# Kernel optimization log

Measured on AMD Instinct MI355X. Metric: run time of the kernel, lower is better.

Reference implementation:

```python
import jax, jax.numpy as jnp
import numpy as np

N = 524288          # number of query points
L_FREQ = 16         # frequencies in positional encoding -> dim_encoding = 3*2*16 = 96
DIM_ENC = 96
DIM_HID = 128
NUM_LAYERS = 8      # 1 input layer + 7 hidden layers + 1 output layer
DIM_OUT = 4
DIM_IN_HID = DIM_HID + DIM_ENC  # concat skip: 224


def setup_inputs() -> dict:
    key = jax.random.key(0)
    ks = jax.random.split(key, 7)
    def lin(k, fan_in, shape):
        return jax.random.uniform(k, shape, jnp.float32, -1.0, 1.0) / np.sqrt(fan_in)
    return {
        "query_points": jax.random.uniform(ks[0], (N, 3), jnp.float32),
        "W0": lin(ks[1], DIM_ENC, (DIM_ENC, DIM_HID)),
        "b0": lin(ks[2], DIM_ENC, (DIM_HID,)),
        "Wh": lin(ks[3], DIM_IN_HID, (NUM_LAYERS - 1, DIM_IN_HID, DIM_HID)),
        "bh": lin(ks[4], DIM_IN_HID, (NUM_LAYERS - 1, DIM_HID)),
        "Wl": lin(ks[5], DIM_IN_HID, (DIM_IN_HID, DIM_OUT)),
        "bl": lin(ks[6], DIM_IN_HID, (DIM_OUT,)),
    }


def _encode(x):
    # NeRF frequency encoding: [N,3] -> [N, 3*2*L_FREQ]
    freqs = (2.0 ** jnp.arange(L_FREQ, dtype=x.dtype)) * jnp.pi
    xf = x[..., None] * freqs                      # [N, 3, L]
    enc = jnp.concatenate([jnp.sin(xf), jnp.cos(xf)], axis=-1)  # [N, 3, 2L]
    return enc.reshape(x.shape[0], -1)             # [N, 96]


def reference(query_points, W0, b0, Wh, bh, Wl, bl):
    enc = _encode(query_points)                    # [N, 96]
    outs = jnp.maximum(enc @ W0 + b0, 0.0)         # [N, 128]
    outs = jnp.concatenate([outs, enc], axis=-1)   # concat skip -> [N, 224]
    for i in range(Wh.shape[0]):                   # 7 structurally-distinct hidden layers
        outs = jnp.maximum(outs @ Wh[i] + bh[i], 0.0)
        outs = jnp.concatenate([outs, enc], axis=-1)
    return outs @ Wl + bl                          # [N, 4], no activation on last layer
```

## Files before the change

kernel.cpp:

```cpp
#include <hip/hip_runtime.h>
#include <stdint.h>

typedef unsigned short u16;
typedef __bf16 bf16x8 __attribute__((ext_vector_type(8)));
typedef float f32x4 __attribute__((ext_vector_type(4)));
typedef float f32x16 __attribute__((ext_vector_type(16)));
typedef unsigned int u32;

#define IMG_H(l) (14336 + ((l)-1) * 30720)
#define IMG_OUT 229376
#define IMG_TOTAL 237056

__device__ inline int fmap(int k) {
    int s = k >> 4, h = (k >> 3) & 1, j = k & 7;
    return 32 * (s >> 1) + 16 * (s & 1) + 8 * (j >> 2) + 4 * h + (j & 3);
}
__device__ inline u16 b16rne(float v) {
    u32 u = __builtin_bit_cast(u32, v);
    u += 0x7FFFu + ((u >> 16) & 1u);
    return (u16)(u >> 16);
}

__global__ void nf_prep(const float* __restrict__ W0, const float* __restrict__ b0,
                        const float* __restrict__ Wh, const float* __restrict__ bh,
                        const float* __restrict__ Wl, const float* __restrict__ bl,
                        u16* __restrict__ img) {
    int idx = blockIdx.x * 256 + threadIdx.x;
    if (idx >= IMG_TOTAL) return;
    float v;
    if (idx < 14336) {
        int gg = idx >> 3, j = idx & 7;
        int koct = gg >> 7, i = gg & 127, k = koct * 8 + j;
        v = (k < 96) ? W0[k * 128 + i] : (k == 96) ? b0[i] : 0.f;
    } else if (idx < IMG_OUT) {
        int r = idx - 14336, l = r / 30720, rr = r % 30720;
        int gg = rr >> 3, j = rr & 7;
        int koct = gg >> 7, i = gg & 127, k = koct * 8 + j;
        const float* W = Wh + l * 224 * 128;
        v = (k < 128) ? W[fmap(k) * 128 + i]
          : (k < 224) ? W[k * 128 + i]
          : (k == 224) ? bh[l * 128 + i] : 0.f;
    } else {
        int r = idx - IMG_OUT;
        int gg = r >> 3, j = r & 7;
        int koct = gg >> 5, i = gg & 31, k = koct * 8 + j;
        v = 0.f;
        if (i < 4)
            v = (k < 128) ? Wl[fmap(k) * 4 + i]
              : (k < 224) ? Wl[k * 4 + i]
              : (k == 224) ? bl[i] : 0.f;
    }
    img[idx] = b16rne(v);
}

__device__ inline f32x16 MF32(bf16x8 a, bf16x8 b, f32x16 c) {
    return __builtin_amdgcn_mfma_f32_32x32x16_bf16(a, b, c, 0, 0, 0);
}
__device__ inline bf16x8 fr4(const u32 (&p)[4]) {
    union { u32 u[4]; bf16x8 v; } x;
    x.u[0] = p[0]; x.u[1] = p[1]; x.u[2] = p[2]; x.u[3] = p[3];
    return x.v;
}
__device__ inline bf16x8 frCB(u32 c0) {
    union { u32 u[4]; bf16x8 v; } x;
    x.u[0] = c0; x.u[1] = 0; x.u[2] = 0; x.u[3] = 0;
    return x.v;
}
__device__ inline bf16x8 ldA(const u16* base, int gi) {
    union { uint4 q; bf16x8 v; } x;
    x.q = *(const uint4*)(base + (gi << 3));
    return x.v;
}
__device__ inline u32 pkbf(float a, float b) {
    u32 ua = __builtin_bit_cast(u32, a) + 0x8000u;
    u32 ub = __builtin_bit_cast(u32, b) + 0x8000u;
    return __builtin_amdgcn_perm(ub, ua, 0x07060302u);
}
__device__ inline void stageA(const u16* gsrc, u16* ldst, int bytes, int wave, int lane) {
    const char* gs = (const char*)gsrc + lane * 16;
    char* ls = (char*)ldst;
    for (int c = wave * 1024; c < bytes; c += 4096)
        __builtin_amdgcn_global_load_lds(
            (const __attribute__((address_space(1))) void*)(gs + c),
            (__attribute__((address_space(3))) void*)(ls + c), 16, 0, 0);
}
__device__ inline void zeroacc(f32x16 (&acc)[4][2]) {
#pragma unroll
    for (int t = 0; t < 4; t++)
#pragma unroll
        for (int n = 0; n < 2; n++)
#pragma unroll
            for (int r = 0; r < 16; r++) acc[t][n][r] = 0.f;
}
__device__ inline void buildH(const f32x16 (&acc)[4][2], u32 (&H)[2][8][4]) {
#pragma unroll
    for (int n = 0; n < 2; n++)
#pragma unroll
        for (int s = 0; s < 8; s++) {
            const int t = s >> 1, rb = (s & 1) * 8;
#pragma unroll
            for (int q = 0; q < 4; q++)
                H[n][s][q] = pkbf(fmaxf(acc[t][n][rb + 2 * q], 0.f),
                                  fmaxf(acc[t][n][rb + 2 * q + 1], 0.f));
        }
}

#define WAITV(N) asm volatile("s_waitcnt vmcnt(" #N ")" ::: "memory")
#define BAR() do { __builtin_amdgcn_s_barrier(); __builtin_amdgcn_sched_barrier(0); } while (0)

__device__ inline void mmRow(const u16* A, int h, int m32, int s,
                             bf16x8 B0, bf16x8 B1, f32x16 (&acc)[4][2]) {
#pragma unroll
    for (int t = 0; t < 4; t++) {
        bf16x8 a = ldA(A, (2 * s + h) * 128 + t * 32 + m32);
        acc[t][0] = MF32(a, B0, acc[t][0]);
        acc[t][1] = MF32(a, B1, acc[t][1]);
    }
}

__device__ inline void cH04(const u16* A, int h, int m32, f32x16 (&acc)[4][2],
                            const u32 (&H)[2][8][4]) {
    __builtin_amdgcn_s_setprio(1);
#pragma unroll
    for (int s = 0; s < 5; s++)
        mmRow(A, h, m32, s, fr4(H[0][s]), fr4(H[1][s]), acc);
    __builtin_amdgcn_s_setprio(0);
}
__device__ inline void cH57E0(const u16* A, int h, int m32, f32x16 (&acc)[4][2],
                              const u32 (&H)[2][8][4], const u32 (&E)[2][3][2][4]) {
    __builtin_amdgcn_s_setprio(1);
    mmRow(A, h, m32, 0, fr4(H[0][5]), fr4(H[1][5]), acc);
    mmRow(A, h, m32, 1, fr4(H[0][6]), fr4(H[1][6]), acc);
    mmRow(A, h, m32, 2, fr4(H[0][7]), fr4(H[1][7]), acc);
    mmRow(A, h, m32, 3, fr4(E[0][0][0]), fr4(E[1][0][0]), acc);
    mmRow(A, h, m32, 4, fr4(E[0][0][1]), fr4(E[1][0][1]), acc);
    __builtin_amdgcn_s_setprio(0);
}
__device__ inline void cE12b(const u16* A, int h, int m32, f32x16 (&acc)[4][2],
                             const u32 (&E)[2][3][2][4], u32 CB0) {
    __builtin_amdgcn_s_setprio(1);
    mmRow(A, h, m32, 0, fr4(E[0][1][0]), fr4(E[1][1][0]), acc);
    mmRow(A, h, m32, 1, fr4(E[0][1][1]), fr4(E[1][1][1]), acc);
    mmRow(A, h, m32, 2, fr4(E[0][2][0]), fr4(E[1][2][0]), acc);
    mmRow(A, h, m32, 3, fr4(E[0][2][1]), fr4(E[1][2][1]), acc);
    mmRow(A, h, m32, 4, frCB(CB0), frCB(CB0), acc);
    __builtin_amdgcn_s_setprio(0);
}
__device__ inline void cL0a(const u16* A, int h, int m32, f32x16 (&acc)[4][2],
                            const u32 (&E)[2][3][2][4]) {
    __builtin_amdgcn_s_setprio(1);
#pragma unroll
    for (int s = 0; s < 5; s++)
        mmRow(A, h, m32, s, fr4(E[0][s >> 1][s & 1]), fr4(E[1][s >> 1][s & 1]), acc);
    __builtin_amdgcn_s_setprio(0);
}
__device__ inline void cL0b(const u16* A, int h, int m32, f32x16 (&acc)[4][2],
                            const u32 (&E)[2][3][2][4], u32 CB0) {
    __builtin_amdgcn_s_setprio(1);
    mmRow(A, h, m32, 0, fr4(E[0][2][1]), fr4(E[1][2][1]), acc);
    mmRow(A, h, m32, 1, frCB(CB0), frCB(CB0), acc);
    __builtin_amdgcn_s_setprio(0);
}

__global__ __launch_bounds__(256, 2) void nf_main(const float* __restrict__ qp,
                                                  const u16* __restrict__ img,
                                                  float* __restrict__ out) {
    __shared__ alignas(16) u16 lds[3][10240];
    const int tid = threadIdx.x, wave = tid >> 6, lane = tid & 63;
    const int m32 = lane & 31, h = lane >> 5;
    const int pbase = blockIdx.x * 256 + wave * 64;

    stageA(img, &lds[0][0], 20480, wave, lane);
    stageA(img + 10240, &lds[1][0], 8192, wave, lane);

    u32 E[2][3][2][4];
    const float sc0 = h ? 128.0f : 0.5f;
#pragma unroll
    for (int n = 0; n < 2; n++)
#pragma unroll
        for (int c = 0; c < 3; c++) {
            float r = qp[(pbase + n * 32 + m32) * 3 + c] * sc0;
            float sn[8], cs[8];
#pragma unroll
            for (int t = 0; t < 8; t++) {
                float fr = __builtin_amdgcn_fractf(r);
                sn[t] = __builtin_amdgcn_sinf(fr);
                cs[t] = __builtin_amdgcn_cosf(fr);
                r = r * 2.0f;
            }
#pragma unroll
            for (int q = 0; q < 4; q++) {
                E[n][c][0][q] = pkbf(sn[2 * q], sn[2 * q + 1]);
                E[n][c][1][q] = pkbf(cs[2 * q], cs[2 * q + 1]);
            }
        }
    const u32 CB0 = (h == 0) ? 0x00003F80u : 0u;

    f32x16 acc[4][2];
    u32 H[2][8][4];
    zeroacc(acc);

    WAITV(2); BAR();
    stageA(img + IMG_H(1), &lds[2][0], 20480, wave, lane);
    cL0a(&lds[0][0], h, m32, acc, E);
    WAITV(5); BAR();
    stageA(img + IMG_H(1) + 10240, &lds[0][0], 20480, wave, lane);
    cL0b(&lds[1][0], h, m32, acc, E, CB0);
    buildH(acc, H);
    WAITV(5); BAR();

#pragma unroll 1
    for (int l = 1; l < 8; l++) {
        const int base = IMG_H(l);
        stageA(img + base + 20480, &lds[1][0], 20480, wave, lane);
        zeroacc(acc);
        cH04(&lds[2][0], h, m32, acc, H);
        WAITV(5); BAR();
        const u16* nsrc = (l < 7) ? (img + IMG_H(l + 1)) : (img + IMG_OUT);
        stageA(nsrc, &lds[2][0], (l < 7) ? 20480 : 15360, wave, lane);
        cH57E0(&lds[0][0], h, m32, acc, H, E);
        if (l < 7) { WAITV(5); } else { WAITV(3); }
        BAR();
        if (l < 7)
            stageA(img + IMG_H(l + 1) + 10240, &lds[0][0], 20480, wave, lane);
        cE12b(&lds[1][0], h, m32, acc, E, CB0);
        buildH(acc, H);
        if (l < 7) { WAITV(5); } else { WAITV(0); }
        BAR();
    }

    f32x16 o0, o1;
#pragma unroll
    for (int r = 0; r < 16; r++) { o0[r] = 0.f; o1[r] = 0.f; }
    __builtin_amdgcn_s_setprio(1);
#pragma unroll
    for (int s = 0; s < 15; s++) {
        bf16x8 B0, B1;
        if (s < 8)       { B0 = fr4(H[0][s]); B1 = fr4(H[1][s]); }
        else if (s < 14) { B0 = fr4(E[0][(s - 8) >> 1][(s - 8) & 1]);
                           B1 = fr4(E[1][(s - 8) >> 1][(s - 8) & 1]); }
        else             { B0 = frCB(CB0); B1 = B0; }
        bf16x8 a = ldA(&lds[2][0], (2 * s + h) * 32 + m32);
        o0 = MF32(a, B0, o0);
        o1 = MF32(a, B1, o1);
    }
    __builtin_amdgcn_s_setprio(0);
    if (h == 0) {
        f32x4 w0 = {o0[0], o0[1], o0[2], o0[3]};
        f32x4 w1 = {o1[0], o1[1], o1[2], o1[3]};
        *(f32x4*)(out + 4 * (pbase + m32)) = w0;
        *(f32x4*)(out + 4 * (pbase + 32 + m32)) = w1;
    }
}

extern "C" void kernel_launch(void* const* d_in, const int* in_sizes, int n_in,
                              void* d_out, int out_size, void* d_ws, size_t ws_size,
                              hipStream_t stream) {
    const float* qp = (const float*)d_in[0];
    const float* W0 = (const float*)d_in[1];
    const float* b0 = (const float*)d_in[2];
    const float* Wh = (const float*)d_in[3];
    const float* bh = (const float*)d_in[4];
    const float* Wl = (const float*)d_in[5];
    const float* bl = (const float*)d_in[6];
    float* out = (float*)d_out;
    u16* img = (u16*)d_ws;

    nf_prep<<<926, 256, 0, stream>>>(W0, b0, Wh, bh, Wl, bl, img);
    nf_main<<<2048, 256, 0, stream>>>(qp, img, out);
}
```

Measured before the change: 261.7 us.

## Halve points per wave to cut registers and run three blocks per CU

Each wave now processes 32 points instead of 64, which halves the accumulator and activation register footprint. Launch bounds go from 2 to 3 blocks per CU and the grid doubles. The weight staging is restructured into 16 KB chunks that rotate through a triple LDS buffer with pointer swaps. It also adds an s_sleep on alternating blocks to stagger their start. The trade-off is that each weight fragment loaded from LDS now feeds one MFMA instead of two, so LDS traffic per FLOP doubles.

```diff
diff --git a/kernel.cpp b/kernel.cpp
--- a/kernel.cpp
+++ b/kernel.cpp
@@ -84,172 +84,162 @@
             (const __attribute__((address_space(1))) void*)(gs + c),
             (__attribute__((address_space(3))) void*)(ls + c), 16, 0, 0);
 }
-__device__ inline void zeroacc(f32x16 (&acc)[4][2]) {
+__device__ inline void zeroacc(f32x16 (&acc)[4]) {
 #pragma unroll
     for (int t = 0; t < 4; t++)
 #pragma unroll
-        for (int n = 0; n < 2; n++)
-#pragma unroll
-            for (int r = 0; r < 16; r++) acc[t][n][r] = 0.f;
-}
-__device__ inline void buildH(const f32x16 (&acc)[4][2], u32 (&H)[2][8][4]) {
-#pragma unroll
-    for (int n = 0; n < 2; n++)
-#pragma unroll
-        for (int s = 0; s < 8; s++) {
-            const int t = s >> 1, rb = (s & 1) * 8;
-#pragma unroll
-            for (int q = 0; q < 4; q++)
-                H[n][s][q] = pkbf(fmaxf(acc[t][n][rb + 2 * q], 0.f),
-                                  fmaxf(acc[t][n][rb + 2 * q + 1], 0.f));
-        }
+        for (int r = 0; r < 16; r++) acc[t][r] = 0.f;
+}
+__device__ inline void buildH(const f32x16 (&acc)[4], u32 (&H)[8][4]) {
+#pragma unroll
+    for (int s = 0; s < 8; s++) {
+        const int t = s >> 1, rb = (s & 1) * 8;
+#pragma unroll
+        for (int q = 0; q < 4; q++)
+            H[s][q] = pkbf(fmaxf(acc[t][rb + 2 * q], 0.f),
+                           fmaxf(acc[t][rb + 2 * q + 1], 0.f));
+    }
 }
 
 #define WAITV(N) asm volatile("s_waitcnt vmcnt(" #N ")" ::: "memory")
 #define BAR() do { __builtin_amdgcn_s_barrier(); __builtin_amdgcn_sched_barrier(0); } while (0)
 
-__device__ inline void mmRow(const u16* A, int h, int m32, int s,
-                             bf16x8 B0, bf16x8 B1, f32x16 (&acc)[4][2]) {
+__device__ inline void mmS(const u16* A, int h, int m32, int sl,
+                           bf16x8 B0, f32x16 (&acc)[4]) {
 #pragma unroll
     for (int t = 0; t < 4; t++) {
-        bf16x8 a = ldA(A, (2 * s + h) * 128 + t * 32 + m32);
-        acc[t][0] = MF32(a, B0, acc[t][0]);
-        acc[t][1] = MF32(a, B1, acc[t][1]);
-    }
-}
-
-__device__ inline void cH04(const u16* A, int h, int m32, f32x16 (&acc)[4][2],
-                            const u32 (&H)[2][8][4]) {
-    __builtin_amdgcn_s_setprio(1);
-#pragma unroll
-    for (int s = 0; s < 5; s++)
-        mmRow(A, h, m32, s, fr4(H[0][s]), fr4(H[1][s]), acc);
-    __builtin_amdgcn_s_setprio(0);
-}
-__device__ inline void cH57E0(const u16* A, int h, int m32, f32x16 (&acc)[4][2],
-                              const u32 (&H)[2][8][4], const u32 (&E)[2][3][2][4]) {
-    __builtin_amdgcn_s_setprio(1);
-    mmRow(A, h, m32, 0, fr4(H[0][5]), fr4(H[1][5]), acc);
-    mmRow(A, h, m32, 1, fr4(H[0][6]), fr4(H[1][6]), acc);
-    mmRow(A, h, m32, 2, fr4(H[0][7]), fr4(H[1][7]), acc);
-    mmRow(A, h, m32, 3, fr4(E[0][0][0]), fr4(E[1][0][0]), acc);
-    mmRow(A, h, m32, 4, fr4(E[0][0][1]), fr4(E[1][0][1]), acc);
-    __builtin_amdgcn_s_setprio(0);
-}
-__device__ inline void cE12b(const u16* A, int h, int m32, f32x16 (&acc)[4][2],
-                             const u32 (&E)[2][3][2][4], u32 CB0) {
-    __builtin_amdgcn_s_setprio(1);
-    mmRow(A, h, m32, 0, fr4(E[0][1][0]), fr4(E[1][1][0]), acc);
-    mmRow(A, h, m32, 1, fr4(E[0][1][1]), fr4(E[1][1][1]), acc);
-    mmRow(A, h, m32, 2, fr4(E[0][2][0]), fr4(E[1][2][0]), acc);
-    mmRow(A, h, m32, 3, fr4(E[0][2][1]), fr4(E[1][2][1]), acc);
-    mmRow(A, h, m32, 4, frCB(CB0), frCB(CB0), acc);
-    __builtin_amdgcn_s_setprio(0);
-}
-__device__ inline void cL0a(const u16* A, int h, int m32, f32x16 (&acc)[4][2],
-                            const u32 (&E)[2][3][2][4]) {
-    __builtin_amdgcn_s_setprio(1);
-#pragma unroll
-    for (int s = 0; s < 5; s++)
-        mmRow(A, h, m32, s, fr4(E[0][s >> 1][s & 1]), fr4(E[1][s >> 1][s & 1]), acc);
-    __builtin_amdgcn_s_setprio(0);
-}
-__device__ inline void cL0b(const u16* A, int h, int m32, f32x16 (&acc)[4][2],
-                            const u32 (&E)[2][3][2][4], u32 CB0) {
-    __builtin_amdgcn_s_setprio(1);
-    mmRow(A, h, m32, 0, fr4(E[0][2][1]), fr4(E[1][2][1]), acc);
-    mmRow(A, h, m32, 1, frCB(CB0), frCB(CB0), acc);
-    __builtin_amdgcn_s_setprio(0);
-}
-
-__global__ __launch_bounds__(256, 2) void nf_main(const float* __restrict__ qp,
+        bf16x8 a = ldA(A, (2 * sl + h) * 128 + t * 32 + m32);
+        acc[t] = MF32(a, B0, acc[t]);
+    }
+}
+
+__device__ inline void phH03(const u16* A, int h, int m32, f32x16 (&acc)[4],
+                             const u32 (&H)[8][4]) {
+    __builtin_amdgcn_s_setprio(1);
+#pragma unroll
+    for (int sl = 0; sl < 4; sl++) mmS(A, h, m32, sl, fr4(H[sl]), acc);
+    __builtin_amdgcn_s_setprio(0);
+}
+__device__ inline void phH47(const u16* A, int h, int m32, f32x16 (&acc)[4],
+                             const u32 (&H)[8][4]) {
+    __builtin_amdgcn_s_setprio(1);
+#pragma unroll
+    for (int sl = 0; sl < 4; sl++) mmS(A, h, m32, sl, fr4(H[4 + sl]), acc);
+    __builtin_amdgcn_s_setprio(0);
+}
+__device__ inline void phE01(const u16* A, int h, int m32, f32x16 (&acc)[4],
+                             const u32 (&E)[3][2][4]) {
+    __builtin_amdgcn_s_setprio(1);
+#pragma unroll
+    for (int sl = 0; sl < 4; sl++)
+        mmS(A, h, m32, sl, fr4(E[sl >> 1][sl & 1]), acc);
+    __builtin_amdgcn_s_setprio(0);
+}
+__device__ inline void phE2b(const u16* A, int h, int m32, f32x16 (&acc)[4],
+                             const u32 (&E)[3][2][4], u32 CB0) {
+    __builtin_amdgcn_s_setprio(1);
+    mmS(A, h, m32, 0, fr4(E[2][0]), acc);
+    mmS(A, h, m32, 1, fr4(E[2][1]), acc);
+    mmS(A, h, m32, 2, frCB(CB0), acc);
+    __builtin_amdgcn_s_setprio(0);
+}
+
+__global__ __launch_bounds__(256, 3) void nf_main(const float* __restrict__ qp,
                                                   const u16* __restrict__ img,
                                                   float* __restrict__ out) {
-    __shared__ alignas(16) u16 lds[3][10240];
+    __shared__ alignas(16) u16 lds[3][8192];
     const int tid = threadIdx.x, wave = tid >> 6, lane = tid & 63;
     const int m32 = lane & 31, h = lane >> 5;
-    const int pbase = blockIdx.x * 256 + wave * 64;
-
-    stageA(img, &lds[0][0], 20480, wave, lane);
-    stageA(img + 10240, &lds[1][0], 8192, wave, lane);
-
-    u32 E[2][3][2][4];
+    const int pbase = blockIdx.x * 128 + wave * 32;
+
+    if ((blockIdx.x ^ (blockIdx.x >> 8)) & 1) __builtin_amdgcn_s_sleep(20);
+
+    u16* p0 = &lds[0][0];
+    u16* p1 = &lds[1][0];
+    u16* p2 = &lds[2][0];
+
+    stageA(img, p0, 16384, wave, lane);
+    stageA(img + 8192, p1, 12288, wave, lane);
+
+    u32 E[3][2][4];
     const float sc0 = h ? 128.0f : 0.5f;
 #pragma unroll
-    for (int n = 0; n < 2; n++)
-#pragma unroll
-        for (int c = 0; c < 3; c++) {
-            float r = qp[(pbase + n * 32 + m32) * 3 + c] * sc0;
-            float sn[8], cs[8];
-#pragma unroll
-            for (int t = 0; t < 8; t++) {
-                float fr = __builtin_amdgcn_fractf(r);
-                sn[t] = __builtin_amdgcn_sinf(fr);
-                cs[t] = __builtin_amdgcn_cosf(fr);
-                r = r * 2.0f;
-            }
-#pragma unroll
-            for (int q = 0; q < 4; q++) {
-                E[n][c][0][q] = pkbf(sn[2 * q], sn[2 * q + 1]);
-                E[n][c][1][q] = pkbf(cs[2 * q], cs[2 * q + 1]);
-            }
+    for (int c = 0; c < 3; c++) {
+        float r = qp[(pbase + m32) * 3 + c] * sc0;
+        float sn[8], cs[8];
+#pragma unroll
+        for (int t = 0; t < 8; t++) {
+            float fr = __builtin_amdgcn_fractf(r);
+            sn[t] = __builtin_amdgcn_sinf(fr);
+            cs[t] = __builtin_amdgcn_cosf(fr);
+            r = r * 2.0f;
         }
+#pragma unroll
+        for (int q = 0; q < 4; q++) {
+            E[c][0][q] = pkbf(sn[2 * q], sn[2 * q + 1]);
+            E[c][1][q] = pkbf(cs[2 * q], cs[2 * q + 1]);
+        }
+    }
     const u32 CB0 = (h == 0) ? 0x00003F80u : 0u;
 
-    f32x16 acc[4][2];
-    u32 H[2][8][4];
+    f32x16 acc[4];
+    u32 H[8][4];
     zeroacc(acc);
 
-    WAITV(2); BAR();
-    stageA(img + IMG_H(1), &lds[2][0], 20480, wave, lane);
-    cL0a(&lds[0][0], h, m32, acc, E);
-    WAITV(5); BAR();
-    stageA(img + IMG_H(1) + 10240, &lds[0][0], 20480, wave, lane);
-    cL0b(&lds[1][0], h, m32, acc, E, CB0);
+    WAITV(3); BAR();
+    stageA(img + IMG_H(1), p2, 16384, wave, lane);
+    phE01(p0, h, m32, acc, E);
+    WAITV(4); BAR();
+    { u16* t = p0; p0 = p1; p1 = p2; p2 = t; }
+    stageA(img + IMG_H(1) + 8192, p2, 16384, wave, lane);
+    phE2b(p0, h, m32, acc, E, CB0);
     buildH(acc, H);
-    WAITV(5); BAR();
+    WAITV(4); BAR();
+    { u16* t = p0; p0 = p1; p1 = p2; p2 = t; }
 
 #pragma unroll 1
     for (int l = 1; l < 8; l++) {
         const int base = IMG_H(l);
-        stageA(img + base + 20480, &lds[1][0], 20480, wave, lane);
+        stageA(img + base + 16384, p2, 16384, wave, lane);
         zeroacc(acc);
-        cH04(&lds[2][0], h, m32, acc, H);
-        WAITV(5); BAR();
-        const u16* nsrc = (l < 7) ? (img + IMG_H(l + 1)) : (img + IMG_OUT);
-        stageA(nsrc, &lds[2][0], (l < 7) ? 20480 : 15360, wave, lane);
-        cH57E0(&lds[0][0], h, m32, acc, H, E);
-        if (l < 7) { WAITV(5); } else { WAITV(3); }
+        phH03(p0, h, m32, acc, H);
+        WAITV(4); BAR();
+        { u16* t = p0; p0 = p1; p1 = p2; p2 = t; }
+        stageA(img + base + 24576, p2, 12288, wave, lane);
+        phH47(p0, h, m32, acc, H);
+        WAITV(3); BAR();
+        { u16* t = p0; p0 = p1; p1 = p2; p2 = t; }
+        if (l < 7) stageA(img + IMG_H(l + 1), p2, 16384, wave, lane);
+        else       stageA(img + IMG_OUT, p2, 15360, wave, lane);
+        phE01(p0, h, m32, acc, E);
+        if (l < 7) { WAITV(4); } else { WAITV(3); }
         BAR();
-        if (l < 7)
-            stageA(img + IMG_H(l + 1) + 10240, &lds[0][0], 20480, wave, lane);
-        cE12b(&lds[1][0], h, m32, acc, E, CB0);
+        { u16* t = p0; p0 = p1; p1 = p2; p2 = t; }
+        if (l < 7) stageA(img + IMG_H(l + 1) + 8192, p2, 16384, wave, lane);
+        phE2b(p0, h, m32, acc, E, CB0);
         buildH(acc, H);
-        if (l < 7) { WAITV(5); } else { WAITV(0); }
+        if (l < 7) { WAITV(4); } else { WAITV(0); }
         BAR();
-    }
-
-    f32x16 o0, o1;
-#pragma unroll
-    for (int r = 0; r < 16; r++) { o0[r] = 0.f; o1[r] = 0.f; }
+        { u16* t = p0; p0 = p1; p1 = p2; p2 = t; }
+    }
+
+    f32x16 o0;
+#pragma unroll
+    for (int r = 0; r < 16; r++) o0[r] = 0.f;
     __builtin_amdgcn_s_setprio(1);
 #pragma unroll
     for (int s = 0; s < 15; s++) {
-        bf16x8 B0, B1;
-        if (s < 8)       { B0 = fr4(H[0][s]); B1 = fr4(H[1][s]); }
-        else if (s < 14) { B0 = fr4(E[0][(s - 8) >> 1][(s - 8) & 1]);
-                           B1 = fr4(E[1][(s - 8) >> 1][(s - 8) & 1]); }
-        else             { B0 = frCB(CB0); B1 = B0; }
-        bf16x8 a = ldA(&lds[2][0], (2 * s + h) * 32 + m32);
+        bf16x8 B0;
+        if (s < 8)       B0 = fr4(H[s]);
+        else if (s < 14) B0 = fr4(E[(s - 8) >> 1][(s - 8) & 1]);
+        else             B0 = frCB(CB0);
+        bf16x8 a = ldA(p0, (2 * s + h) * 32 + m32);
         o0 = MF32(a, B0, o0);
-        o1 = MF32(a, B1, o1);
     }
     __builtin_amdgcn_s_setprio(0);
     if (h == 0) {
         f32x4 w0 = {o0[0], o0[1], o0[2], o0[3]};
-        f32x4 w1 = {o1[0], o1[1], o1[2], o1[3]};
         *(f32x4*)(out + 4 * (pbase + m32)) = w0;
-        *(f32x4*)(out + 4 * (pbase + 32 + m32)) = w1;
     }
 }
 
@@ -267,5 +257,5 @@
     u16* img = (u16*)d_ws;
 
     nf_prep<<<926, 256, 0, stream>>>(W0, b0, Wh, bh, Wl, bl, img);
-    nf_main<<<2048, 256, 0, stream>>>(qp, img, out);
-}
+    nf_main<<<4096, 256, 0, stream>>>(qp, img, out);
+}
```

New measurement: 291.9 us. 1.12x slower.

## Shrink blocks to two waves with finer rotating triple-buffered weight staging

Applied to the files above, without the earlier changes.

Blocks drop from four waves to two, doubling the grid. Weight staging is split into smaller 12KB chunks of three k-slices, held in a rotating three-buffer LDS ring via pointer swaps, with the output layer also staged in chunks. The aim is to cut LDS per block so more blocks fit per CU and to overlap loads more finely, at the cost of more barriers and twice as many total weight loads into LDS across the grid.

```diff
diff --git a/kernel.cpp b/kernel.cpp
--- a/kernel.cpp
+++ b/kernel.cpp
@@ -76,10 +76,10 @@
     u32 ub = __builtin_bit_cast(u32, b) + 0x8000u;
     return __builtin_amdgcn_perm(ub, ua, 0x07060302u);
 }
-__device__ inline void stageA(const u16* gsrc, u16* ldst, int bytes, int wave, int lane) {
+__device__ inline void stage2(const u16* gsrc, u16* ldst, int bytes, int wave, int lane) {
     const char* gs = (const char*)gsrc + lane * 16;
     char* ls = (char*)ldst;
-    for (int c = wave * 1024; c < bytes; c += 4096)
+    for (int c = wave * 1024; c < bytes; c += 2048)
         __builtin_amdgcn_global_load_lds(
             (const __attribute__((address_space(1))) void*)(gs + c),
             (__attribute__((address_space(3))) void*)(ls + c), 16, 0, 0);
@@ -107,6 +107,7 @@
 
 #define WAITV(N) asm volatile("s_waitcnt vmcnt(" #N ")" ::: "memory")
 #define BAR() do { __builtin_amdgcn_s_barrier(); __builtin_amdgcn_sched_barrier(0); } while (0)
+#define ROT() do { u16* _t = p0; p0 = p1; p1 = p2; p2 = _t; } while (0)
 
 __device__ inline void mmRow(const u16* A, int h, int m32, int s,
                              bf16x8 B0, bf16x8 B1, f32x16 (&acc)[4][2]) {
@@ -117,61 +118,36 @@
         acc[t][1] = MF32(a, B1, acc[t][1]);
     }
 }
-
-__device__ inline void cH04(const u16* A, int h, int m32, f32x16 (&acc)[4][2],
-                            const u32 (&H)[2][8][4]) {
-    __builtin_amdgcn_s_setprio(1);
-#pragma unroll
-    for (int s = 0; s < 5; s++)
-        mmRow(A, h, m32, s, fr4(H[0][s]), fr4(H[1][s]), acc);
-    __builtin_amdgcn_s_setprio(0);
-}
-__device__ inline void cH57E0(const u16* A, int h, int m32, f32x16 (&acc)[4][2],
-                              const u32 (&H)[2][8][4], const u32 (&E)[2][3][2][4]) {
-    __builtin_amdgcn_s_setprio(1);
-    mmRow(A, h, m32, 0, fr4(H[0][5]), fr4(H[1][5]), acc);
-    mmRow(A, h, m32, 1, fr4(H[0][6]), fr4(H[1][6]), acc);
-    mmRow(A, h, m32, 2, fr4(H[0][7]), fr4(H[1][7]), acc);
-    mmRow(A, h, m32, 3, fr4(E[0][0][0]), fr4(E[1][0][0]), acc);
-    mmRow(A, h, m32, 4, fr4(E[0][0][1]), fr4(E[1][0][1]), acc);
-    __builtin_amdgcn_s_setprio(0);
-}
-__device__ inline void cE12b(const u16* A, int h, int m32, f32x16 (&acc)[4][2],
-                             const u32 (&E)[2][3][2][4], u32 CB0) {
-    __builtin_amdgcn_s_setprio(1);
-    mmRow(A, h, m32, 0, fr4(E[0][1][0]), fr4(E[1][1][0]), acc);
-    mmRow(A, h, m32, 1, fr4(E[0][1][1]), fr4(E[1][1][1]), acc);
-    mmRow(A, h, m32, 2, fr4(E[0][2][0]), fr4(E[1][2][0]), acc);
-    mmRow(A, h, m32, 3, fr4(E[0][2][1]), fr4(E[1][2][1]), acc);
-    mmRow(A, h, m32, 4, frCB(CB0), frCB(CB0), acc);
-    __builtin_amdgcn_s_setprio(0);
-}
-__device__ inline void cL0a(const u16* A, int h, int m32, f32x16 (&acc)[4][2],
-                            const u32 (&E)[2][3][2][4]) {
-    __builtin_amdgcn_s_setprio(1);
-#pragma unroll
-    for (int s = 0; s < 5; s++)
-        mmRow(A, h, m32, s, fr4(E[0][s >> 1][s & 1]), fr4(E[1][s >> 1][s & 1]), acc);
-    __builtin_amdgcn_s_setprio(0);
-}
-__device__ inline void cL0b(const u16* A, int h, int m32, f32x16 (&acc)[4][2],
-                            const u32 (&E)[2][3][2][4], u32 CB0) {
-    __builtin_amdgcn_s_setprio(1);
-    mmRow(A, h, m32, 0, fr4(E[0][2][1]), fr4(E[1][2][1]), acc);
-    mmRow(A, h, m32, 1, frCB(CB0), frCB(CB0), acc);
-    __builtin_amdgcn_s_setprio(0);
-}
-
-__global__ __launch_bounds__(256, 2) void nf_main(const float* __restrict__ qp,
+__device__ inline void ph3(const u16* A, int h, int m32, f32x16 (&acc)[4][2],
+                           bf16x8 Ba0, bf16x8 Ba1, bf16x8 Bb0, bf16x8 Bb1,
+                           bf16x8 Bc0, bf16x8 Bc1) {
+    __builtin_amdgcn_s_setprio(1);
+    mmRow(A, h, m32, 0, Ba0, Ba1, acc);
+    mmRow(A, h, m32, 1, Bb0, Bb1, acc);
+    mmRow(A, h, m32, 2, Bc0, Bc1, acc);
+    __builtin_amdgcn_s_setprio(0);
+}
+__device__ inline void ph1(const u16* A, int h, int m32, f32x16 (&acc)[4][2],
+                           bf16x8 B) {
+    __builtin_amdgcn_s_setprio(1);
+    mmRow(A, h, m32, 0, B, B, acc);
+    __builtin_amdgcn_s_setprio(0);
+}
+
+__global__ __launch_bounds__(128, 2) void nf_main(const float* __restrict__ qp,
                                                   const u16* __restrict__ img,
                                                   float* __restrict__ out) {
-    __shared__ alignas(16) u16 lds[3][10240];
+    __shared__ alignas(16) u16 lds[3][6144];
     const int tid = threadIdx.x, wave = tid >> 6, lane = tid & 63;
     const int m32 = lane & 31, h = lane >> 5;
-    const int pbase = blockIdx.x * 256 + wave * 64;
-
-    stageA(img, &lds[0][0], 20480, wave, lane);
-    stageA(img + 10240, &lds[1][0], 8192, wave, lane);
+    const int pbase = blockIdx.x * 128 + wave * 64;
+
+    u16* p0 = &lds[0][0];
+    u16* p1 = &lds[1][0];
+    u16* p2 = &lds[2][0];
+
+    stage2(img, p0, 12288, wave, lane);
+    stage2(img + 6144, p1, 12288, wave, lane);
 
     u32 E[2][3][2][4];
     const float sc0 = h ? 128.0f : 0.5f;
@@ -200,47 +176,84 @@
     u32 H[2][8][4];
     zeroacc(acc);
 
-    WAITV(2); BAR();
-    stageA(img + IMG_H(1), &lds[2][0], 20480, wave, lane);
-    cL0a(&lds[0][0], h, m32, acc, E);
-    WAITV(5); BAR();
-    stageA(img + IMG_H(1) + 10240, &lds[0][0], 20480, wave, lane);
-    cL0b(&lds[1][0], h, m32, acc, E, CB0);
+    WAITV(6); BAR();
+    stage2(img + 12288, p2, 4096, wave, lane);
+    ph3(p0, h, m32, acc, fr4(E[0][0][0]), fr4(E[1][0][0]),
+        fr4(E[0][0][1]), fr4(E[1][0][1]), fr4(E[0][1][0]), fr4(E[1][1][0]));
+    WAITV(2); BAR(); ROT();
+    stage2(img + IMG_H(1), p2, 12288, wave, lane);
+    ph3(p0, h, m32, acc, fr4(E[0][1][1]), fr4(E[1][1][1]),
+        fr4(E[0][2][0]), fr4(E[1][2][0]), fr4(E[0][2][1]), fr4(E[1][2][1]));
+    WAITV(6); BAR(); ROT();
+    stage2(img + IMG_H(1) + 6144, p2, 12288, wave, lane);
+    ph1(p0, h, m32, acc, frCB(CB0));
     buildH(acc, H);
-    WAITV(5); BAR();
+    WAITV(6); BAR(); ROT();
 
 #pragma unroll 1
     for (int l = 1; l < 8; l++) {
         const int base = IMG_H(l);
-        stageA(img + base + 20480, &lds[1][0], 20480, wave, lane);
+        stage2(img + base + 12288, p2, 12288, wave, lane);
         zeroacc(acc);
-        cH04(&lds[2][0], h, m32, acc, H);
-        WAITV(5); BAR();
-        const u16* nsrc = (l < 7) ? (img + IMG_H(l + 1)) : (img + IMG_OUT);
-        stageA(nsrc, &lds[2][0], (l < 7) ? 20480 : 15360, wave, lane);
-        cH57E0(&lds[0][0], h, m32, acc, H, E);
-        if (l < 7) { WAITV(5); } else { WAITV(3); }
-        BAR();
-        if (l < 7)
-            stageA(img + IMG_H(l + 1) + 10240, &lds[0][0], 20480, wave, lane);
-        cE12b(&lds[1][0], h, m32, acc, E, CB0);
+        ph3(p0, h, m32, acc, fr4(H[0][0]), fr4(H[1][0]),
+            fr4(H[0][1]), fr4(H[1][1]), fr4(H[0][2]), fr4(H[1][2]));
+        WAITV(6); BAR(); ROT();
+        stage2(img + base + 18432, p2, 12288, wave, lane);
+        ph3(p0, h, m32, acc, fr4(H[0][3]), fr4(H[1][3]),
+            fr4(H[0][4]), fr4(H[1][4]), fr4(H[0][5]), fr4(H[1][5]));
+        WAITV(6); BAR(); ROT();
+        stage2(img + base + 24576, p2, 12288, wave, lane);
+        ph3(p0, h, m32, acc, fr4(H[0][6]), fr4(H[1][6]),
+            fr4(H[0][7]), fr4(H[1][7]), fr4(E[0][0][0]), fr4(E[1][0][0]));
+        WAITV(6); BAR(); ROT();
+        if (l < 7) stage2(img + IMG_H(l + 1), p2, 12288, wave, lane);
+        else       stage2(img + IMG_OUT, p2, 6144, wave, lane);
+        ph3(p0, h, m32, acc, fr4(E[0][0][1]), fr4(E[1][0][1]),
+            fr4(E[0][1][0]), fr4(E[1][1][0]), fr4(E[0][1][1]), fr4(E[1][1][1]));
+        if (l < 7) { WAITV(6); } else { WAITV(3); }
+        BAR(); ROT();
+        if (l < 7) stage2(img + IMG_H(l + 1) + 6144, p2, 12288, wave, lane);
+        else       stage2(img + IMG_OUT + 3072, p2, 6144, wave, lane);
+        ph3(p0, h, m32, acc, fr4(E[0][2][0]), fr4(E[1][2][0]),
+            fr4(E[0][2][1]), fr4(E[1][2][1]), frCB(CB0), frCB(CB0));
         buildH(acc, H);
-        if (l < 7) { WAITV(5); } else { WAITV(0); }
-        BAR();
+        if (l < 7) { WAITV(6); } else { WAITV(3); }
+        BAR(); ROT();
     }
 
     f32x16 o0, o1;
 #pragma unroll
     for (int r = 0; r < 16; r++) { o0[r] = 0.f; o1[r] = 0.f; }
-    __builtin_amdgcn_s_setprio(1);
-#pragma unroll
-    for (int s = 0; s < 15; s++) {
+    stage2(img + IMG_OUT + 6144, p2, 3072, wave, lane);
+    __builtin_amdgcn_s_setprio(1);
+#pragma unroll
+    for (int s = 0; s < 6; s++) {
+        bf16x8 a = ldA(p0, (2 * s + h) * 32 + m32);
+        o0 = MF32(a, fr4(H[0][s]), o0);
+        o1 = MF32(a, fr4(H[1][s]), o1);
+    }
+    __builtin_amdgcn_s_setprio(0);
+    WAITV(1); BAR(); ROT();
+    __builtin_amdgcn_s_setprio(1);
+#pragma unroll
+    for (int s = 0; s < 6; s++) {
         bf16x8 B0, B1;
-        if (s < 8)       { B0 = fr4(H[0][s]); B1 = fr4(H[1][s]); }
-        else if (s < 14) { B0 = fr4(E[0][(s - 8) >> 1][(s - 8) & 1]);
-                           B1 = fr4(E[1][(s - 8) >> 1][(s - 8) & 1]); }
-        else             { B0 = frCB(CB0); B1 = B0; }
-        bf16x8 a = ldA(&lds[2][0], (2 * s + h) * 32 + m32);
+        if (s < 2)      { B0 = fr4(H[0][6 + s]);        B1 = fr4(H[1][6 + s]); }
+        else            { B0 = fr4(E[0][(s-2)>>1][(s-2)&1]);
+                          B1 = fr4(E[1][(s-2)>>1][(s-2)&1]); }
+        bf16x8 a = ldA(p0, (2 * s + h) * 32 + m32);
+        o0 = MF32(a, B0, o0);
+        o1 = MF32(a, B1, o1);
+    }
+    __builtin_amdgcn_s_setprio(0);
+    WAITV(0); BAR(); ROT();
+    __builtin_amdgcn_s_setprio(1);
+#pragma unroll
+    for (int s = 0; s < 3; s++) {
+        bf16x8 B0, B1;
+        if (s < 2) { B0 = fr4(E[0][2][s]); B1 = fr4(E[1][2][s]); }
+        else       { B0 = frCB(CB0);       B1 = B0; }
+        bf16x8 a = ldA(p0, (2 * s + h) * 32 + m32);
         o0 = MF32(a, B0, o0);
         o1 = MF32(a, B1, o1);
     }
@@ -267,5 +280,5 @@
     u16* img = (u16*)d_ws;
 
     nf_prep<<<926, 256, 0, stream>>>(W0, b0, Wh, bh, Wl, bl, img);
-    nf_main<<<2048, 256, 0, stream>>>(qp, img, out);
-}
+    nf_main<<<4096, 128, 0, stream>>>(qp, img, out);
+}
```

Result: slower. 313.7 us (+19.9%).
